# Kernel tuning notes

Hardware: AMD Instinct MI355X
Metric: run time of the kernel (lower is better)

The kernel has to match this reference:

```python
import jax, jax.numpy as jnp
import numpy as np

N = 30000   # nodes
E = 480000  # edges
C = 64      # in_channels
NC = 101    # num_classes
K1 = 5      # kernel_size per dim
K = K1 * K1 # 25 kernel weight matrices (dim=2)


def _spline_conv(x, src, dst, pseudo, W, root, bias):
    """SplineConv, degree-1 open B-spline, dim=2, kernel_size=5, aggr='mean'.
    x: [N,C_in], pseudo: [E,2] in [0,1], W: [25,C_in,C_out], root: [C_in,C_out].
    """
    n, c = x.shape
    v = pseudo * (K1 - 1)                       # [E,2] in [0, K1-1]
    bot = jnp.clip(jnp.floor(v), 0, K1 - 1)
    frac = v - bot                              # fractional part
    bot_i = bot.astype(jnp.int32)
    bits = jnp.array([[0, 0], [0, 1], [1, 0], [1, 1]], dtype=jnp.int32)  # S=4 combos
    idx_d = jnp.clip(bot_i[:, None, :] + bits[None, :, :], 0, K1 - 1)    # [E,4,2]
    w_d = jnp.where(bits[None, :, :] == 1, frac[:, None, :], 1.0 - frac[:, None, :])
    B = w_d[..., 0] * w_d[..., 1]               # [E,4] basis weights
    kidx = idx_d[..., 0] * K1 + idx_d[..., 1]   # [E,4] flat kernel index in [0,25)
    msg = B[:, :, None] * x[src][:, None, :]    # [E,4,C] weighted source feats
    seg = (dst[:, None] * K + kidx).reshape(-1) # combined (node,kernel) segment id
    acc = jax.ops.segment_sum(msg.reshape(-1, c), seg, num_segments=n * K)
    acc = acc.reshape(n, K, c)                  # [N,25,C]
    out = jnp.einsum('nkc,kcd->nd', acc, W)     # apply kernel weight matrices
    deg = jax.ops.segment_sum(jnp.ones(dst.shape[0], x.dtype), dst, num_segments=n)
    out = out / jnp.maximum(deg, 1.0)[:, None]  # mean aggregation
    out = out + x @ root                        # root weight
    if bias is not None:
        out = out + bias
    return out


def _bn(x, g, b):
    m = x.mean(0)
    v = x.var(0)
    return g * (x - m) * jax.lax.rsqrt(v + 1e-5) + b


def setup_inputs() -> dict:
    key = jax.random.key(0)
    ks = jax.random.split(key, 30)
    p = lambda k, shape: jax.random.normal(k, shape, jnp.float32) * 0.05
    d = {
        'x': jax.random.normal(ks[0], (N, C), jnp.float32),
        'edge_attr': jax.random.uniform(ks[1], (E, 3), dtype=jnp.float32),
        'src': jax.random.randint(ks[2], (E,), 0, N),
        'dst': jax.random.randint(ks[3], (E,), 0, N),
    }
    for i, name in enumerate(['conv1', 'conv2', 'conv3']):
        d[name + '_W'] = p(ks[4 + 2 * i], (K, C, C))
        d[name + '_root'] = p(ks[5 + 2 * i], (C, C))
        d['norm%d_gamma' % (i + 1)] = jnp.ones((C,), jnp.float32)
        d['norm%d_beta' % (i + 1)] = jnp.zeros((C,), jnp.float32)
    for j, (name, oc) in enumerate([('regr', 4), ('cls', NC), ('obj', 1)]):
        d[name + '_W'] = p(ks[10 + 3 * j], (K, C, oc))
        d[name + '_root'] = p(ks[11 + 3 * j], (C, oc))
        d[name + '_bias'] = jnp.zeros((oc,), jnp.float32)
    return d


def reference(x, edge_attr, src, dst,
              conv1_W, conv1_root, norm1_gamma, norm1_beta,
              conv2_W, conv2_root, norm2_gamma, norm2_beta,
              conv3_W, conv3_root, norm3_gamma, norm3_beta,
              regr_W, regr_root, regr_bias,
              cls_W, cls_root, cls_bias,
              obj_W, obj_root, obj_bias):
    pseudo = edge_attr[:, :2]
    x1 = jax.nn.relu(_bn(_spline_conv(x, src, dst, pseudo, conv1_W, conv1_root, None), norm1_gamma, norm1_beta))
    x2 = jax.nn.relu(_bn(_spline_conv(x1, src, dst, pseudo, conv2_W, conv2_root, None), norm2_gamma, norm2_beta))
    x3 = jax.nn.relu(_bn(_spline_conv(x1, src, dst, pseudo, conv3_W, conv3_root, None), norm3_gamma, norm3_beta))
    reg = _spline_conv(x2, src, dst, pseudo, regr_W, regr_root, regr_bias)
    cls = _spline_conv(x3, src, dst, pseudo, cls_W, cls_root, cls_bias)
    obj = _spline_conv(x3, src, dst, pseudo, obj_W, obj_root, obj_bias)
    return (cls, reg, obj)
```

## Files before the change

kernel.cpp:

```cpp
#include <hip/hip_runtime.h>
#include <hip/hip_bf16.h>

#define NN 30000
#define NE 480000
#define CIN 64
#define KD 1600
#define KT 1664
#define KMAC 13
#define BM 64
#define NBLK 469
#define MROWS (NBLK*BM)
#define NBS 118
#define REG_OFF  (30000*101)
#define OBJ_OFF  (30000*105)

typedef short bf16x8 __attribute__((ext_vector_type(8)));
typedef float f32x4  __attribute__((ext_vector_type(4)));
typedef __attribute__((address_space(3))) unsigned lds_u32;
typedef __attribute__((address_space(1))) const unsigned glb_u32;

__device__ __forceinline__ ushort f2bf(float x) {
    union { float f; unsigned u; } v; v.f = x;
    unsigned r = v.u + 0x7FFFu + ((v.u >> 16) & 1u);
    return (ushort)(r >> 16);
}
__device__ __forceinline__ float bf2f(ushort u) {
    union { unsigned i; float f; } v; v.i = ((unsigned)u) << 16; return v.f;
}
__device__ __forceinline__ float bflo(unsigned u) {
    union { unsigned i; float f; } v; v.i = u << 16; return v.f;
}
__device__ __forceinline__ float bfhi(unsigned u) {
    union { unsigned i; float f; } v; v.i = u & 0xFFFF0000u; return v.f;
}

#define WAITV2 asm volatile("s_waitcnt vmcnt(2)" ::: "memory")
#define WAITV0 asm volatile("s_waitcnt vmcnt(0)" ::: "memory")

__global__ void k_count(const int* __restrict__ dst, int* __restrict__ deg) {
    int e = blockIdx.x * 256 + threadIdx.x;
    if (e < NE) atomicAdd(&deg[dst[e]], 1);
}

__global__ void k_scan1(const int* __restrict__ deg, int* __restrict__ bsum) {
    __shared__ int sred[4];
    int i = blockIdx.x * 256 + threadIdx.x;
    int v = (i < NN) ? deg[i] : 0;
    #pragma unroll
    for (int o = 32; o >= 1; o >>= 1) v += __shfl_down(v, o);
    int w = threadIdx.x >> 6, l = threadIdx.x & 63;
    if (l == 0) sred[w] = v;
    __syncthreads();
    if (threadIdx.x == 0) bsum[blockIdx.x] = sred[0] + sred[1] + sred[2] + sred[3];
}

__global__ void k_scan2(const int* __restrict__ bsum, int* __restrict__ boff) {
    __shared__ int s[128];
    int t = threadIdx.x;
    int v = (t < NBS) ? bsum[t] : 0;
    s[t] = v; __syncthreads();
    for (int o = 1; o < 128; o <<= 1) {
        int u = (t >= o) ? s[t - o] : 0;
        __syncthreads(); s[t] += u; __syncthreads();
    }
    if (t < NBS) boff[t] = s[t] - v;
}

__global__ void k_scan3(const int* __restrict__ deg, const int* __restrict__ boff,
                        int* __restrict__ rp, int* __restrict__ cur, float* __restrict__ invd) {
    __shared__ int s[256];
    int t = threadIdx.x;
    int i = blockIdx.x * 256 + t;
    int v = (i < NN) ? deg[i] : 0;
    s[t] = v; __syncthreads();
    for (int o = 1; o < 256; o <<= 1) {
        int u = (t >= o) ? s[t - o] : 0;
        __syncthreads(); s[t] += u; __syncthreads();
    }
    int ex = s[t] - v + boff[blockIdx.x];
    if (i < NN) {
        rp[i] = ex; cur[i] = ex;
        invd[i] = 1.f / (float)(v > 0 ? v : 1);
    }
    if (i == NN - 1) rp[NN] = NE;
}

__global__ void k_scatter(const float* __restrict__ ea, const int* __restrict__ src,
                          const int* __restrict__ dst, int* __restrict__ cur,
                          const float* __restrict__ invd, uint4* __restrict__ mE) {
    int e = blockIdx.x * 256 + threadIdx.x;
    if (e >= NE) return;
    float p0 = ea[e*3+0], p1 = ea[e*3+1];
    float v0 = p0*4.f, v1 = p1*4.f;
    float b0 = fminf(fmaxf(floorf(v0),0.f),4.f);
    float b1 = fminf(fmaxf(floorf(v1),0.f),4.f);
    float f0 = v0-b0, f1 = v1-b1;
    int i0 = (int)b0, i1 = (int)b1;
    int dn = dst[e];
    float s = invd[dn];
    float B00 = (1.f-f0)*(1.f-f1)*s;
    float B01 = (1.f-f0)*f1*s;
    float B10 = f0*(1.f-f1)*s;
    float B11 = f0*f1*s;
    int k00 = i0*5 + i1;
    int pos = atomicAdd(&cur[dn], 1);
    unsigned w01 = (unsigned)f2bf(B00) | ((unsigned)f2bf(B01) << 16);
    unsigned w23 = (unsigned)f2bf(B10) | ((unsigned)f2bf(B11) << 16);
    mE[pos] = make_uint4((unsigned)k00 | ((unsigned)src[e] << 8), w01, w23, 0u);
}

__global__ void k_prepw(const float* W1,const float* R1,const float* W2,const float* R2,
                        const float* W3,const float* R3,const float* Wr,const float* Rr,
                        const float* Wc,const float* Rc,const float* Wo,const float* Ro,
                        ushort* T1, ushort* T23, ushort* Tr, ushort* TcTo) {
    int b = blockIdx.x;
    const float* W; const float* R; ushort* T; int od; int col;
    if      (b < 64)  { W=W1; R=R1; T=T1  + (long)b*KT;       od=64;  col=b;     }
    else if (b < 128) { W=W2; R=R2; T=T23 + (long)(b-64)*KT;  od=64;  col=b-64;  }
    else if (b < 192) { W=W3; R=R3; T=T23 + (long)(b-64)*KT;  od=64;  col=b-128; }
    else if (b < 208) { W=Wr; R=Rr; T=Tr  + (long)(b-192)*KT; od=4;   col=b-192; }
    else if (b < 320) { W=Wc; R=Rc; T=TcTo+ (long)(b-208)*KT; od=101; col=b-208; }
    else              { W=Wo; R=Ro; T=TcTo+ (long)(b-208)*KT; od=1;   col=b-320; }
    for (int kc = threadIdx.x; kc < KT; kc += 256) {
        float v = 0.f;
        if (col < od) v = (kc < KD) ? W[(long)kc*od + col] : R[(long)(kc-KD)*od + col];
        T[kc] = f2bf(v);
    }
}

__global__ void k_cvt(const float* __restrict__ x, ushort* __restrict__ xb) {
    int idx = blockIdx.x * 1024 + threadIdx.x;
    if (idx < NN*CIN) xb[idx] = f2bf(x[idx]);
}

__global__ void k_norm(const float* __restrict__ y, const float* __restrict__ st,
                       const float* __restrict__ g, const float* __restrict__ be,
                       ushort* __restrict__ xb) {
    int idx = blockIdx.x * 1024 + threadIdx.x;
    if (idx >= NN*CIN) return;
    int d = idx & 63;
    const float inv_n = 1.f / (float)NN;
    float m = st[d] * inv_n;
    float var = st[64 + d] * inv_n - m * m;
    float a = g[d] * rsqrtf(var + 1e-5f);
    float c = be[d] - m * a;
    xb[idx] = f2bf(fmaxf(y[idx] * a + c, 0.f));
}

#define AGGC(K, A_, B_, C_, D_) case K: A_ += b0v*xu; B_ += b1v*xu; C_ += b2v*xu; D_ += b3v*xu; break;

__global__ void k_agg(
                      const int* __restrict__ rp, const uint4* __restrict__ mE,
                      const ushort* __restrict__ f, ushort* __restrict__ A) {
    int wid = (blockIdx.x * 256 + threadIdx.x) >> 6;
    wid = __builtin_amdgcn_readfirstlane(wid);
    int l = threadIdx.x & 63;
    if (wid >= NN) return;
    float a00=0.f,a01=0.f,a02=0.f,a03=0.f,a04=0.f;
    float a05=0.f,a06=0.f,a07=0.f,a08=0.f,a09=0.f;
    float a10=0.f,a11=0.f,a12=0.f,a13=0.f,a14=0.f;
    float a15=0.f,a16=0.f,a17=0.f,a18=0.f,a19=0.f;
    float a20=0.f,a21=0.f,a22=0.f,a23=0.f,a24=0.f;
    int beg = rp[wid], end = rp[wid + 1];
    for (int e0 = beg; e0 < end; e0 += 8) {
        uint4 m[8];
        #pragma unroll
        for (int u = 0; u < 8; ++u) {
            int e = e0 + u;
            m[u] = mE[(e < end) ? e : beg];
            if (e >= end) { m[u].y = 0u; m[u].z = 0u; }
        }
        ushort xv[8];
        #pragma unroll
        for (int u = 0; u < 8; ++u) xv[u] = f[(long)(m[u].x >> 8) * CIN + l];
        __builtin_amdgcn_sched_barrier(0);
        #pragma unroll
        for (int u = 0; u < 8; ++u) {
            float xu = bf2f(xv[u]);
            float b0v = bflo(m[u].y), b1v = bfhi(m[u].y);
            float b2v = bflo(m[u].z), b3v = bfhi(m[u].z);
            int k00 = __builtin_amdgcn_readfirstlane(m[u].x & 0xFFu);
            switch (k00) {
                AGGC(0,  a00,a01,a05,a06)
                AGGC(1,  a01,a02,a06,a07)
                AGGC(2,  a02,a03,a07,a08)
                AGGC(3,  a03,a04,a08,a09)
                AGGC(5,  a05,a06,a10,a11)
                AGGC(6,  a06,a07,a11,a12)
                AGGC(7,  a07,a08,a12,a13)
                AGGC(8,  a08,a09,a13,a14)
                AGGC(10, a10,a11,a15,a16)
                AGGC(11, a11,a12,a16,a17)
                AGGC(12, a12,a13,a17,a18)
                AGGC(13, a13,a14,a18,a19)
                AGGC(15, a15,a16,a20,a21)
                AGGC(16, a16,a17,a21,a22)
                AGGC(17, a17,a18,a22,a23)
                AGGC(18, a18,a19,a23,a24)
                default: break;
            }
        }
    }
    ushort* rb = A + (long)wid * KT + l;
    #define STO(K, V) rb[K*CIN] = f2bf(V);
    STO(0,a00)  STO(1,a01)  STO(2,a02)  STO(3,a03)  STO(4,a04)
    STO(5,a05)  STO(6,a06)  STO(7,a07)  STO(8,a08)  STO(9,a09)
    STO(10,a10) STO(11,a11) STO(12,a12) STO(13,a13) STO(14,a14)
    STO(15,a15) STO(16,a16) STO(17,a17) STO(18,a18) STO(19,a19)
    STO(20,a20) STO(21,a21) STO(22,a22) STO(23,a23) STO(24,a24)
    #undef STO
    rb[KD] = f[(long)wid * CIN + l];
}

template<int MODE>
__global__ void k_gemm(const ushort* __restrict__ A, const ushort* __restrict__ B,
                       float* __restrict__ o0, float* __restrict__ o1,
                       float* __restrict__ s0, float* __restrict__ s1,
                       const float* __restrict__ b0, const float* __restrict__ b1) {
    __shared__ ushort As[3 * 8192];
    f32x4* part = (f32x4*)As;
    const int tid = threadIdx.x, w = tid >> 6, l = tid & 63;
    const int m0 = blockIdx.x * BM;

    int colrow;
    if constexpr (MODE == 0)      colrow = ((w & 3) << 4) + (l & 15);
    else if constexpr (MODE == 2) colrow = (l & 15);
    else                          colrow = (w << 4) + (l & 15);
    const ushort* Bp = B + (long)colrow * KT + ((l >> 4) << 3);

    const int row0 = (w << 3) + (l >> 4);
    const int row1 = row0 + 4;
    const ushort* g0 = A + (long)(m0 + row0) * KT + (((l & 15) ^ (row0 & 7)) << 3);
    const ushort* g1 = A + (long)(m0 + row1) * KT + (((l & 15) ^ (row1 & 7)) << 3);
    ushort* d0 = (ushort*)As + (w << 10);
    ushort* d1 = d0 + 512;

    auto stage = [&](int ks, int bf) {
        const ushort* sA = g0 + ks * 128;
        const ushort* sB = g1 + ks * 128;
        __builtin_amdgcn_global_load_lds((glb_u32*)sA, (lds_u32*)(d0 + bf * 8192), 16, 0, 0);
        __builtin_amdgcn_global_load_lds((glb_u32*)sB, (lds_u32*)(d1 + bf * 8192), 16, 0, 0);
    };

    f32x4 acc[4];
    #pragma unroll
    for (int m = 0; m < 4; ++m) acc[m] = (f32x4){0.f,0.f,0.f,0.f};

    stage(0, 0);
    stage(1, 1);
    WAITV2;
    __builtin_amdgcn_s_barrier();
    __builtin_amdgcn_sched_barrier(0);

    for (int ks = 0; ks < KMAC; ++ks) {
        const int bufc = ks % 3;
        bool act;
        if constexpr (MODE == 0)      act = (w < 4) ? (ks < 7) : (ks >= 7);
        else if constexpr (MODE == 2) act = ((ks & 7) == w);
        else                          act = true;
        if (act) {
            bf16x8 bb[4];
            #pragma unroll
            for (int s = 0; s < 4; ++s) bb[s] = *(const bf16x8*)(Bp + ks * 128 + s * 32);
            if (ks + 2 < KMAC) stage(ks + 2, (ks + 2) % 3);
            const char* Ab = (const char*)As + bufc * 16384;
            #pragma unroll
            for (int s = 0; s < 4; ++s) {
                #pragma unroll
                for (int m = 0; m < 4; ++m) {
                    int r = (m << 4) + (l & 15);
                    int j = (s << 2) + (l >> 4);
                    bf16x8 a = *(const bf16x8*)(Ab + r * 256 + ((j ^ (r & 7)) << 4));
                    acc[m] = __builtin_amdgcn_mfma_f32_16x16x32_bf16(a, bb[s], acc[m], 0, 0, 0);
                }
            }
        } else {
            if (ks + 2 < KMAC) stage(ks + 2, (ks + 2) % 3);
        }
        if (ks < KMAC - 2) { WAITV2; } else { WAITV0; }
        __builtin_amdgcn_s_barrier();
        __builtin_amdgcn_sched_barrier(0);
    }

    auto emit = [&](f32x4* ac, float* out, int ostride, int col, int odcap, float bv, float* stats) {
        float p1 = 0.f, p2 = 0.f;
        #pragma unroll
        for (int m = 0; m < 4; ++m) {
            #pragma unroll
            for (int r = 0; r < 4; ++r) {
                int row = m0 + (m << 4) + ((l >> 4) << 2) + r;
                if (row < NN) {
                    float v = ac[m][r] + bv;
                    if (col < odcap) out[(long)row * ostride + col] = v;
                    p1 += v; p2 += v * v;
                }
            }
        }
        if (stats) {
            p1 += __shfl_down(p1, 32); p2 += __shfl_down(p2, 32);
            p1 += __shfl_down(p1, 16); p2 += __shfl_down(p2, 16);
            if (l < 16) { atomicAdd(&stats[col], p1); atomicAdd(&stats[64 + col], p2); }
        }
    };

    if constexpr (MODE == 0) {
        if (w >= 4) {
            #pragma unroll
            for (int m = 0; m < 4; ++m) part[((w & 3) << 8) + (l << 2) + m] = acc[m];
        }
        __syncthreads();
        if (w < 4) {
            #pragma unroll
            for (int m = 0; m < 4; ++m) acc[m] += part[((w & 3) << 8) + (l << 2) + m];
            emit(acc, o0, 64, ((w & 3) << 4) + (l & 15), 64, 0.f, s0);
        }
    } else if constexpr (MODE == 1) {
        if (w < 4) emit(acc, o0, 64, (w << 4) + (l & 15), 64, 0.f, s0);
        else       emit(acc, o1, 64, ((w - 4) << 4) + (l & 15), 64, 0.f, s1);
    } else if constexpr (MODE == 2) {
        if (w > 0) {
            #pragma unroll
            for (int m = 0; m < 4; ++m) part[((w - 1) << 8) + (l << 2) + m] = acc[m];
        }
        __syncthreads();
        if (w == 0) {
            for (int i = 0; i < 7; ++i) {
                #pragma unroll
                for (int m = 0; m < 4; ++m) acc[m] += part[(i << 8) + (l << 2) + m];
            }
            int col = l & 15;
            emit(acc, o0, 4, col, 4, (col < 4) ? b0[col] : 0.f, nullptr);
        }
    } else {
        if (w < 7) {
            int col = (w << 4) + (l & 15);
            emit(acc, o0, 101, col, 101, (col < 101) ? b0[col] : 0.f, nullptr);
        } else {
            int col = l & 15;
            emit(acc, o1, 1, col, 1, b1[0], nullptr);
        }
    }
}

extern "C" void kernel_launch(void* const* d_in, const int* in_sizes, int n_in,
                              void* d_out, int out_size, void* d_ws, size_t ws_size,
                              hipStream_t stream) {
    const float* x    = (const float*)d_in[0];
    const float* ea   = (const float*)d_in[1];
    const int*   src  = (const int*)d_in[2];
    const int*   dst  = (const int*)d_in[3];
    const float* W1   = (const float*)d_in[4];
    const float* R1   = (const float*)d_in[5];
    const float* g1   = (const float*)d_in[6];
    const float* be1  = (const float*)d_in[7];
    const float* W2   = (const float*)d_in[8];
    const float* R2   = (const float*)d_in[9];
    const float* g2   = (const float*)d_in[10];
    const float* be2  = (const float*)d_in[11];
    const float* W3   = (const float*)d_in[12];
    const float* R3   = (const float*)d_in[13];
    const float* g3   = (const float*)d_in[14];
    const float* be3  = (const float*)d_in[15];
    const float* Wr   = (const float*)d_in[16];
    const float* Rr   = (const float*)d_in[17];
    const float* br   = (const float*)d_in[18];
    const float* Wc   = (const float*)d_in[19];
    const float* Rc   = (const float*)d_in[20];
    const float* bc   = (const float*)d_in[21];
    const float* Wo   = (const float*)d_in[22];
    const float* Ro   = (const float*)d_in[23];
    const float* bo   = (const float*)d_in[24];
    float* out = (float*)d_out;

    char* p = (char*)d_ws;
    auto alloc = [&](size_t bytes) { char* r = p; p += (bytes + 255) & ~(size_t)255; return r; };
    uint4*  mE   = (uint4*) alloc((size_t)NE * 16);
    int*    deg  = (int*)   alloc((size_t)NN * 4);
    int*    rp   = (int*)   alloc((size_t)(NN + 1) * 4);
    int*    cur  = (int*)   alloc((size_t)NN * 4);
    float*  invd = (float*) alloc((size_t)NN * 4);
    int*    bsum = (int*)   alloc((size_t)NBS * 4);
    int*    boff = (int*)   alloc((size_t)NBS * 4);
    ushort* T1   = (ushort*)alloc((size_t)64  * KT * 2);
    ushort* T23  = (ushort*)alloc((size_t)128 * KT * 2);
    ushort* Tr   = (ushort*)alloc((size_t)16  * KT * 2);
    ushort* TcTo = (ushort*)alloc((size_t)128 * KT * 2);
    float*  y1   = (float*) alloc((size_t)NN * CIN * 4);
    float*  y2   = (float*) alloc((size_t)NN * CIN * 4);
    float*  y3   = (float*) alloc((size_t)NN * CIN * 4);
    ushort* xb   = (ushort*)alloc((size_t)NN * CIN * 2);
    float*  stats= (float*) alloc(3 * 128 * 4);
    ushort* A    = (ushort*)alloc((size_t)MROWS * KT * 2);
    float* st1 = stats, *st2 = stats + 128, *st3 = stats + 256;

    hipMemsetAsync(deg, 0, (size_t)NN * 4, stream);
    hipMemsetAsync(stats, 0, 3 * 128 * 4, stream);

    k_count  <<<1875, 256, 0, stream>>>(dst, deg);
    k_scan1  <<<NBS, 256, 0, stream>>>(deg, bsum);
    k_scan2  <<<1, 128, 0, stream>>>(bsum, boff);
    k_scan3  <<<NBS, 256, 0, stream>>>(deg, boff, rp, cur, invd);
    k_scatter<<<1875, 256, 0, stream>>>(ea, src, dst, cur, invd, mE);
    k_prepw  <<<336, 256, 0, stream>>>(W1,R1,W2,R2,W3,R3,Wr,Rr,Wc,Rc,Wo,Ro,T1,T23,Tr,TcTo);
    k_cvt    <<<1875, 1024, 0, stream>>>(x, xb);

    k_agg    <<<7500, 256, 0, stream>>>(rp, mE, xb, A);
    k_gemm<0><<<NBLK, 512, 0, stream>>>(A, T1, y1, nullptr, st1, nullptr, nullptr, nullptr);
    k_norm   <<<1875, 1024, 0, stream>>>(y1, st1, g1, be1, xb);
    k_agg    <<<7500, 256, 0, stream>>>(rp, mE, xb, A);
    k_gemm<1><<<NBLK, 512, 0, stream>>>(A, T23, y2, y3, st2, st3, nullptr, nullptr);
    k_norm   <<<1875, 1024, 0, stream>>>(y2, st2, g2, be2, xb);
    k_agg    <<<7500, 256, 0, stream>>>(rp, mE, xb, A);
    k_gemm<2><<<NBLK, 512, 0, stream>>>(A, Tr, out + REG_OFF, nullptr, nullptr, nullptr, br, nullptr);
    k_norm   <<<1875, 1024, 0, stream>>>(y3, st3, g3, be3, xb);
    k_agg    <<<7500, 256, 0, stream>>>(rp, mE, xb, A);
    k_gemm<3><<<NBLK, 512, 0, stream>>>(A, TcTo, out, out + OBJ_OFF, nullptr, nullptr, bc, bo);
}
```

Before: 404.7 us.

## Fuse batch-norm and ReLU into aggregation gather, store pre-norm outputs as bf16

```diff
diff --git a/kernel.cpp b/kernel.cpp
--- a/kernel.cpp
+++ b/kernel.cpp
@@ -133,29 +133,26 @@
     if (idx < NN*CIN) xb[idx] = f2bf(x[idx]);
 }
 
-__global__ void k_norm(const float* __restrict__ y, const float* __restrict__ st,
-                       const float* __restrict__ g, const float* __restrict__ be,
-                       ushort* __restrict__ xb) {
-    int idx = blockIdx.x * 1024 + threadIdx.x;
-    if (idx >= NN*CIN) return;
-    int d = idx & 63;
-    const float inv_n = 1.f / (float)NN;
-    float m = st[d] * inv_n;
-    float var = st[64 + d] * inv_n - m * m;
-    float a = g[d] * rsqrtf(var + 1e-5f);
-    float c = be[d] - m * a;
-    xb[idx] = f2bf(fmaxf(y[idx] * a + c, 0.f));
-}
-
 #define AGGC(K, A_, B_, C_, D_) case K: A_ += b0v*xu; B_ += b1v*xu; C_ += b2v*xu; D_ += b3v*xu; break;
 
+template<bool NORM>
 __global__ void k_agg(
                       const int* __restrict__ rp, const uint4* __restrict__ mE,
-                      const ushort* __restrict__ f, ushort* __restrict__ A) {
+                      const ushort* __restrict__ f,
+                      const float* __restrict__ st, const float* __restrict__ g,
+                      const float* __restrict__ be, ushort* __restrict__ A) {
     int wid = (blockIdx.x * 256 + threadIdx.x) >> 6;
     wid = __builtin_amdgcn_readfirstlane(wid);
     int l = threadIdx.x & 63;
     if (wid >= NN) return;
+    float na = 0.f, nc = 0.f;
+    if (NORM) {
+        const float inv_n = 1.f / (float)NN;
+        float mm = st[l] * inv_n;
+        float var = st[64 + l] * inv_n - mm * mm;
+        float rs = rsqrtf(var + 1e-5f);
+        na = g[l] * rs; nc = be[l] - mm * na;
+    }
     float a00=0.f,a01=0.f,a02=0.f,a03=0.f,a04=0.f;
     float a05=0.f,a06=0.f,a07=0.f,a08=0.f,a09=0.f;
     float a10=0.f,a11=0.f,a12=0.f,a13=0.f,a14=0.f;
@@ -177,6 +174,7 @@
         #pragma unroll
         for (int u = 0; u < 8; ++u) {
             float xu = bf2f(xv[u]);
+            if (NORM) xu = fmaxf(xu * na + nc, 0.f);
             float b0v = bflo(m[u].y), b1v = bfhi(m[u].y);
             float b2v = bflo(m[u].z), b3v = bfhi(m[u].z);
             int k00 = __builtin_amdgcn_readfirstlane(m[u].x & 0xFFu);
@@ -209,12 +207,16 @@
     STO(15,a15) STO(16,a16) STO(17,a17) STO(18,a18) STO(19,a19)
     STO(20,a20) STO(21,a21) STO(22,a22) STO(23,a23) STO(24,a24)
     #undef STO
-    rb[KD] = f[(long)wid * CIN + l];
+    {
+        float rv = bf2f(f[(long)wid * CIN + l]);
+        if (NORM) rv = fmaxf(rv * na + nc, 0.f);
+        rb[KD] = f2bf(rv);
+    }
 }
 
 template<int MODE>
 __global__ void k_gemm(const ushort* __restrict__ A, const ushort* __restrict__ B,
-                       float* __restrict__ o0, float* __restrict__ o1,
+                       void* __restrict__ o0v, void* __restrict__ o1v,
                        float* __restrict__ s0, float* __restrict__ s1,
                        const float* __restrict__ b0, const float* __restrict__ b1) {
     __shared__ ushort As[3 * 8192];
@@ -282,7 +284,18 @@
         __builtin_amdgcn_sched_barrier(0);
     }
 
-    auto emit = [&](f32x4* ac, float* out, int ostride, int col, int odcap, float bv, float* stats) {
+    auto emitf = [&](f32x4* ac, float* out, int ostride, int col, int odcap, float bv) {
+        #pragma unroll
+        for (int m = 0; m < 4; ++m) {
+            #pragma unroll
+            for (int r = 0; r < 4; ++r) {
+                int row = m0 + (m << 4) + ((l >> 4) << 2) + r;
+                if (row < NN && col < odcap)
+                    out[(long)row * ostride + col] = ac[m][r] + bv;
+            }
+        }
+    };
+    auto emitb = [&](f32x4* ac, ushort* out, int col, float* stats) {
         float p1 = 0.f, p2 = 0.f;
         #pragma unroll
         for (int m = 0; m < 4; ++m) {
@@ -290,17 +303,15 @@
             for (int r = 0; r < 4; ++r) {
                 int row = m0 + (m << 4) + ((l >> 4) << 2) + r;
                 if (row < NN) {
-                    float v = ac[m][r] + bv;
-                    if (col < odcap) out[(long)row * ostride + col] = v;
+                    float v = ac[m][r];
+                    out[(long)row * 64 + col] = f2bf(v);
                     p1 += v; p2 += v * v;
                 }
             }
         }
-        if (stats) {
-            p1 += __shfl_down(p1, 32); p2 += __shfl_down(p2, 32);
-            p1 += __shfl_down(p1, 16); p2 += __shfl_down(p2, 16);
-            if (l < 16) { atomicAdd(&stats[col], p1); atomicAdd(&stats[64 + col], p2); }
-        }
+        p1 += __shfl_down(p1, 32); p2 += __shfl_down(p2, 32);
+        p1 += __shfl_down(p1, 16); p2 += __shfl_down(p2, 16);
+        if (l < 16) { atomicAdd(&stats[col], p1); atomicAdd(&stats[64 + col], p2); }
     };
 
     if constexpr (MODE == 0) {
@@ -312,11 +323,11 @@
         if (w < 4) {
             #pragma unroll
             for (int m = 0; m < 4; ++m) acc[m] += part[((w & 3) << 8) + (l << 2) + m];
-            emit(acc, o0, 64, ((w & 3) << 4) + (l & 15), 64, 0.f, s0);
+            emitb(acc, (ushort*)o0v, ((w & 3) << 4) + (l & 15), s0);
         }
     } else if constexpr (MODE == 1) {
-        if (w < 4) emit(acc, o0, 64, (w << 4) + (l & 15), 64, 0.f, s0);
-        else       emit(acc, o1, 64, ((w - 4) << 4) + (l & 15), 64, 0.f, s1);
+        if (w < 4) emitb(acc, (ushort*)o0v, (w << 4) + (l & 15), s0);
+        else       emitb(acc, (ushort*)o1v, ((w - 4) << 4) + (l & 15), s1);
     } else if constexpr (MODE == 2) {
         if (w > 0) {
             #pragma unroll
@@ -329,15 +340,15 @@
                 for (int m = 0; m < 4; ++m) acc[m] += part[(i << 8) + (l << 2) + m];
             }
             int col = l & 15;
-            emit(acc, o0, 4, col, 4, (col < 4) ? b0[col] : 0.f, nullptr);
+            emitf(acc, (float*)o0v, 4, col, 4, (col < 4) ? b0[col] : 0.f);
         }
     } else {
         if (w < 7) {
             int col = (w << 4) + (l & 15);
-            emit(acc, o0, 101, col, 101, (col < 101) ? b0[col] : 0.f, nullptr);
+            emitf(acc, (float*)o0v, 101, col, 101, (col < 101) ? b0[col] : 0.f);
         } else {
             int col = l & 15;
-            emit(acc, o1, 1, col, 1, b1[0], nullptr);
+            emitf(acc, (float*)o1v, 1, col, 1, b1[0]);
         }
     }
 }
@@ -385,10 +396,10 @@
     ushort* T23  = (ushort*)alloc((size_t)128 * KT * 2);
     ushort* Tr   = (ushort*)alloc((size_t)16  * KT * 2);
     ushort* TcTo = (ushort*)alloc((size_t)128 * KT * 2);
-    float*  y1   = (float*) alloc((size_t)NN * CIN * 4);
-    float*  y2   = (float*) alloc((size_t)NN * CIN * 4);
-    float*  y3   = (float*) alloc((size_t)NN * CIN * 4);
     ushort* xb   = (ushort*)alloc((size_t)NN * CIN * 2);
+    ushort* yb1  = (ushort*)alloc((size_t)NN * CIN * 2);
+    ushort* yb2  = (ushort*)alloc((size_t)NN * CIN * 2);
+    ushort* yb3  = (ushort*)alloc((size_t)NN * CIN * 2);
     float*  stats= (float*) alloc(3 * 128 * 4);
     ushort* A    = (ushort*)alloc((size_t)MROWS * KT * 2);
     float* st1 = stats, *st2 = stats + 128, *st3 = stats + 256;
@@ -404,15 +415,12 @@
     k_prepw  <<<336, 256, 0, stream>>>(W1,R1,W2,R2,W3,R3,Wr,Rr,Wc,Rc,Wo,Ro,T1,T23,Tr,TcTo);
     k_cvt    <<<1875, 1024, 0, stream>>>(x, xb);
 
-    k_agg    <<<7500, 256, 0, stream>>>(rp, mE, xb, A);
-    k_gemm<0><<<NBLK, 512, 0, stream>>>(A, T1, y1, nullptr, st1, nullptr, nullptr, nullptr);
-    k_norm   <<<1875, 1024, 0, stream>>>(y1, st1, g1, be1, xb);
-    k_agg    <<<7500, 256, 0, stream>>>(rp, mE, xb, A);
-    k_gemm<1><<<NBLK, 512, 0, stream>>>(A, T23, y2, y3, st2, st3, nullptr, nullptr);
-    k_norm   <<<1875, 1024, 0, stream>>>(y2, st2, g2, be2, xb);
-    k_agg    <<<7500, 256, 0, stream>>>(rp, mE, xb, A);
+    k_agg<false><<<7500, 256, 0, stream>>>(rp, mE, xb, nullptr, nullptr, nullptr, A);
+    k_gemm<0><<<NBLK, 512, 0, stream>>>(A, T1, yb1, nullptr, st1, nullptr, nullptr, nullptr);
+    k_agg<true><<<7500, 256, 0, stream>>>(rp, mE, yb1, st1, g1, be1, A);
+    k_gemm<1><<<NBLK, 512, 0, stream>>>(A, T23, yb2, yb3, st2, st3, nullptr, nullptr);
+    k_agg<true><<<7500, 256, 0, stream>>>(rp, mE, yb2, st2, g2, be2, A);
     k_gemm<2><<<NBLK, 512, 0, stream>>>(A, Tr, out + REG_OFF, nullptr, nullptr, nullptr, br, nullptr);
-    k_norm   <<<1875, 1024, 0, stream>>>(y3, st3, g3, be3, xb);
-    k_agg    <<<7500, 256, 0, stream>>>(rp, mE, xb, A);
+    k_agg<true><<<7500, 256, 0, stream>>>(rp, mE, yb3, st3, g3, be3, A);
     k_gemm<3><<<NBLK, 512, 0, stream>>>(A, TcTo, out, out + OBJ_OFF, nullptr, nullptr, bc, bo);
 }
```

Result: faster. 387.5 us, median of 2 (-4.3%).
